# Performance work log

Measured on AMD Instinct MI355X. Metric: run time of the kernel, lower is better.

Reference implementation:

```python
import jax, jax.numpy as jnp
import numpy as np

N_NODES = 100000
N_EDGES = 1600000
D_IN = 64
D_OUT = 64


def setup_inputs() -> dict:
    key = jax.random.key(0)
    k1, k2, k3, k4, k5 = jax.random.split(key, 5)
    x = jax.random.normal(k1, (N_NODES, D_IN), dtype=jnp.float32)
    edge_src = jax.random.randint(k2, (N_EDGES,), 0, N_NODES, dtype=jnp.int32)
    edge_dst = jax.random.randint(k3, (N_EDGES,), 0, N_NODES, dtype=jnp.int32)
    edge_val = jnp.ones((N_EDGES,), dtype=jnp.float32)
    stdv = 1.0 / np.sqrt(D_OUT)
    weight = jax.random.uniform(k4, (D_IN, D_OUT), minval=-stdv, maxval=stdv, dtype=jnp.float32)
    epsilon = jnp.ones((1,), dtype=jnp.float32)
    bias = jax.random.uniform(k5, (D_OUT,), minval=-stdv, maxval=stdv, dtype=jnp.float32)
    return {"x": x, "edge_src": edge_src, "edge_dst": edge_dst,
            "edge_val": edge_val, "weight": weight, "epsilon": epsilon, "bias": bias}


def reference(x, edge_src, edge_dst, edge_val, weight, epsilon, bias):
    # spmm(adj, x): row i of adj gathers neighbors -> segment_sum over edge_src
    # adj[i, j] = edge_val for edge (src=i, dst=j)
    msgs = edge_val[:, None] * x[edge_dst]            # [E, D_in]
    agg = jax.ops.segment_sum(msgs, edge_src, num_segments=N_NODES)  # [N, D_in]
    # epsilon * eye(N) @ x == epsilon * x (avoid O(N^2) identity)
    rep = agg + epsilon * x                            # [N, D_in]
    out = rep @ weight + bias                          # [N, D_out]
    return out, rep
```

## Files before the change

### kernel.cpp

```cpp
#include <hip/hip_runtime.h>
#include <hip/hip_fp16.h>

#define N_NODES 100000
#define N_EDGES 1600000
#define D 64

#define NB 391
#define BLKA 391
#define EPB 4096
#define GST 400

#define WS_GHIST   0
#define WS_G       156416
#define WS_ROWPTR  156832
#define WS_PAIRSU  256864
#define WS_XH      1856864

__global__ __launch_bounds__(512) void k_hist_cvt(
    const int* __restrict__ esrc, const float* __restrict__ x,
    int* __restrict__ ghist, uint2* __restrict__ xh2)
{
    __shared__ int h[NB];
    int t = threadIdx.x, blk = blockIdx.x;
    if (t < NB) h[t] = 0;
    __syncthreads();
    int base = blk * EPB;
    #pragma unroll
    for (int i = 0; i < 2; ++i) {
        int e0 = base + i * 2048 + t * 4;
        if (e0 < N_EDGES) {
            int4 s4 = *(const int4*)(esrc + e0);
            atomicAdd(&h[s4.x >> 8], 1);
            atomicAdd(&h[s4.y >> 8], 1);
            atomicAdd(&h[s4.z >> 8], 1);
            atomicAdd(&h[s4.w >> 8], 1);
        }
    }
    {
        const float4* x4 = (const float4*)x;
        #pragma unroll
        for (int i = 0; i < 8; ++i) {
            int f = blk * 4096 + i * 512 + t;
            if (f < N_NODES * (D / 4)) {
                float4 v = x4[f];
                uint2 o;
                o.x = (unsigned int)__half_as_ushort(__float2half_rn(v.x)) |
                      ((unsigned int)__half_as_ushort(__float2half_rn(v.y)) << 16);
                o.y = (unsigned int)__half_as_ushort(__float2half_rn(v.z)) |
                      ((unsigned int)__half_as_ushort(__float2half_rn(v.w)) << 16);
                xh2[f] = o;
            }
        }
    }
    __syncthreads();
    if (t < NB) ghist[blk * GST + t] = h[t];
}

__global__ __launch_bounds__(512) void k_scatter(
    const int* __restrict__ esrc, const int* __restrict__ edst,
    const float* __restrict__ eval_, const int* __restrict__ ghist,
    int* __restrict__ G, int2* __restrict__ tpairs)
{
    __shared__ int base[NB];
    __shared__ int wsum[8];
    int t = threadIdx.x, blk = blockIdx.x;
    int lane = t & 63, wid = t >> 6;

    int tot = 0, P = 0;
    if (t < NB) {
        int c = 0;
        for (; c + 16 <= BLKA; c += 16) {
            int v[16];
            #pragma unroll
            for (int k = 0; k < 16; ++k) v[k] = ghist[(c + k) * GST + t];
            #pragma unroll
            for (int k = 0; k < 16; ++k) {
                tot += v[k];
                P += ((c + k) < blk) ? v[k] : 0;
            }
        }
        for (; c < BLKA; ++c) {
            int v = ghist[c * GST + t];
            tot += v;
            P += (c < blk) ? v : 0;
        }
    }
    int s = tot;
    #pragma unroll
    for (int off = 1; off < 64; off <<= 1) {
        int y = __shfl_up(s, off, 64);
        if (lane >= off) s += y;
    }
    if (lane == 63) wsum[wid] = s;
    __syncthreads();
    if (t == 0) {
        int r = 0;
        #pragma unroll
        for (int k = 0; k < 8; ++k) { int v = wsum[k]; wsum[k] = r; r += v; }
    }
    __syncthreads();
    int Gv = wsum[wid] + s - tot;
    if (t < NB) {
        base[t] = Gv + P;
        if (blk == 0) {
            G[t] = Gv;
            if (t == NB - 1) G[NB] = Gv + tot;
        }
    }
    __syncthreads();

    int eb = blk * EPB;
    #pragma unroll
    for (int i = 0; i < 2; ++i) {
        int e0 = eb + i * 2048 + t * 4;
        if (e0 < N_EDGES) {
            int4 s4 = *(const int4*)(esrc + e0);
            int4 d4 = *(const int4*)(edst + e0);
            float4 v4 = *(const float4*)(eval_ + e0);
            int p0 = atomicAdd(&base[s4.x >> 8], 1);
            int p1 = atomicAdd(&base[s4.y >> 8], 1);
            int p2 = atomicAdd(&base[s4.z >> 8], 1);
            int p3 = atomicAdd(&base[s4.w >> 8], 1);
            tpairs[p0] = make_int2(((s4.x & 255) << 17) | d4.x, __float_as_int(v4.x));
            tpairs[p1] = make_int2(((s4.y & 255) << 17) | d4.y, __float_as_int(v4.y));
            tpairs[p2] = make_int2(((s4.z & 255) << 17) | d4.z, __float_as_int(v4.z));
            tpairs[p3] = make_int2(((s4.w & 255) << 17) | d4.w, __float_as_int(v4.w));
        }
    }
}

__global__ __launch_bounds__(512) void k_build(
    const int2* __restrict__ tpairs, const int* __restrict__ G,
    int* __restrict__ row_ptr, unsigned int* __restrict__ pairsu)
{
    __shared__ int hist[256], cursor[256], wsum4[4];
    int b = blockIdx.x, t = threadIdx.x;
    int s_begin = G[b];
    int s_end   = G[b + 1];
    if (t < 256) hist[t] = 0;
    __syncthreads();
    #pragma unroll 4
    for (int pos = s_begin + t; pos < s_end; pos += 512)
        atomicAdd(&hist[(tpairs[pos].x >> 17) & 255], 1);
    __syncthreads();
    int lane = t & 63, wid = t >> 6;
    if (t < 256) {
        int v = hist[t], s = v;
        #pragma unroll
        for (int off = 1; off < 64; off <<= 1) {
            int y = __shfl_up(s, off, 64);
            if (lane >= off) s += y;
        }
        if (lane == 63) wsum4[wid] = s;
        __syncthreads();
        if (t == 0) {
            int r = 0;
            #pragma unroll
            for (int k = 0; k < 4; ++k) { int w = wsum4[k]; wsum4[k] = r; r += w; }
        }
        __syncthreads();
        int excl = wsum4[wid] + s - v;
        cursor[t] = excl;
        int node = (b << 8) + t;
        if (node <= N_NODES) row_ptr[node] = s_begin + excl;
    } else {
        __syncthreads();
        __syncthreads();
    }
    __syncthreads();
    #pragma unroll 4
    for (int pos = s_begin + t; pos < s_end; pos += 512) {
        int2 pv = tpairs[pos];
        int k = (pv.x >> 17) & 255;
        int p = atomicAdd(&cursor[k], 1);
        unsigned int dst = (unsigned int)pv.x & 0x1FFFFu;
        unsigned int hb = (unsigned int)__half_as_ushort(
            __float2half_rn(__int_as_float(pv.y)));
        pairsu[s_begin + p] = (dst << 15) | (hb >> 1);
    }
}

#define GATHER_BLOCKS 2048

__global__ __launch_bounds__(256) void k_gather(
    const uint4* __restrict__ xh4, const int* __restrict__ row_ptr,
    const unsigned int* __restrict__ pairsu, const float* __restrict__ epsilon,
    float* __restrict__ rep)
{
    int w = (blockIdx.x * 256 + threadIdx.x) >> 6;
    int nw = gridDim.x * 4;
    int lane = threadIdx.x & 63;
    int sub = lane >> 3;
    int h8 = lane & 7;
    float eps = epsilon[0];

    int r0 = (int)((long long)w * N_NODES / nw);
    int r1 = (int)((long long)(w + 1) * N_NODES / nw);

    for (int row = r0; row < r1; ++row) {
        int start = __builtin_amdgcn_readfirstlane(row_ptr[row]);
        int end   = __builtin_amdgcn_readfirstlane(row_ptr[row + 1]);
        float4 accA = make_float4(0.f, 0.f, 0.f, 0.f);
        float4 accB = make_float4(0.f, 0.f, 0.f, 0.f);
        for (int j = start; j < end; j += 32) {
            unsigned int pk[4]; uint4 a[4];
            #pragma unroll
            for (int u = 0; u < 4; ++u) {
                int e = j + u * 8 + sub;
                pk[u] = (e < end) ? pairsu[e] : 0u;
            }
            #pragma unroll
            for (int u = 0; u < 4; ++u)
                a[u] = xh4[(size_t)(pk[u] >> 15) * 8 + h8];
            #pragma unroll
            for (int u = 0; u < 4; ++u) {
                unsigned short hb = (unsigned short)((pk[u] & 0x7FFFu) << 1);
                float vv = __half2float(__ushort_as_half(hb));
                float2 f0 = __half22float2(*reinterpret_cast<const __half2*>(&a[u].x));
                float2 f1 = __half22float2(*reinterpret_cast<const __half2*>(&a[u].y));
                float2 f2 = __half22float2(*reinterpret_cast<const __half2*>(&a[u].z));
                float2 f3 = __half22float2(*reinterpret_cast<const __half2*>(&a[u].w));
                accA.x += vv * f0.x; accA.y += vv * f0.y;
                accA.z += vv * f1.x; accA.w += vv * f1.y;
                accB.x += vv * f2.x; accB.y += vv * f2.y;
                accB.z += vv * f3.x; accB.w += vv * f3.y;
            }
        }
        #pragma unroll
        for (int off = 8; off <= 32; off <<= 1) {
            accA.x += __shfl_xor(accA.x, off, 64);
            accA.y += __shfl_xor(accA.y, off, 64);
            accA.z += __shfl_xor(accA.z, off, 64);
            accA.w += __shfl_xor(accA.w, off, 64);
            accB.x += __shfl_xor(accB.x, off, 64);
            accB.y += __shfl_xor(accB.y, off, 64);
            accB.z += __shfl_xor(accB.z, off, 64);
            accB.w += __shfl_xor(accB.w, off, 64);
        }
        if (lane < 8) {
            uint4 xr = xh4[(size_t)row * 8 + lane];
            float2 x0 = __half22float2(*reinterpret_cast<const __half2*>(&xr.x));
            float2 x1 = __half22float2(*reinterpret_cast<const __half2*>(&xr.y));
            float2 x2 = __half22float2(*reinterpret_cast<const __half2*>(&xr.z));
            float2 x3 = __half22float2(*reinterpret_cast<const __half2*>(&xr.w));
            float4* r4 = (float4*)rep;
            r4[(size_t)row * 16 + lane * 2] =
                make_float4(accA.x + eps * x0.x, accA.y + eps * x0.y,
                            accA.z + eps * x1.x, accA.w + eps * x1.y);
            r4[(size_t)row * 16 + lane * 2 + 1] =
                make_float4(accB.x + eps * x2.x, accB.y + eps * x2.y,
                            accB.z + eps * x3.x, accB.w + eps * x3.y);
        }
    }
}

#define GEMM_TM 64
__global__ __launch_bounds__(256) void k_gemm(
    const float* __restrict__ rep, const float* __restrict__ weight,
    const float* __restrict__ bias, float* __restrict__ out)
{
    __shared__ float rep_s[GEMM_TM * 68];
    __shared__ float Ws[D * D];
    int t = threadIdx.x;
    {
        const float4* w4 = (const float4*)weight;
        float4* s4 = (float4*)Ws;
        #pragma unroll
        for (int i = 0; i < (D * D / 4) / 256; ++i)
            s4[t + i * 256] = w4[t + i * 256];
    }
    int row0 = blockIdx.x * GEMM_TM;
    {
        const float4* r4 = (const float4*)rep;
        #pragma unroll
        for (int i = 0; i < 4; ++i) {
            int f = t + i * 256;
            int rr = f >> 4, kk4 = f & 15;
            float4 v = (row0 + rr < N_NODES) ? r4[(size_t)(row0 + rr) * 16 + kk4]
                                             : make_float4(0.f, 0.f, 0.f, 0.f);
            rep_s[rr * 68 + kk4 * 4 + 0] = v.x;
            rep_s[rr * 68 + kk4 * 4 + 1] = v.y;
            rep_s[rr * 68 + kk4 * 4 + 2] = v.z;
            rep_s[rr * 68 + kk4 * 4 + 3] = v.w;
        }
    }
    __syncthreads();

    int tx = t & 15, ty = t >> 4;
    float4 b4 = ((const float4*)bias)[tx];
    float acc[4][4];
    #pragma unroll
    for (int i = 0; i < 4; ++i) {
        acc[i][0] = b4.x; acc[i][1] = b4.y; acc[i][2] = b4.z; acc[i][3] = b4.w;
    }
    #pragma unroll 4
    for (int k4 = 0; k4 < 16; ++k4) {
        float4 rv[4];
        #pragma unroll
        for (int i = 0; i < 4; ++i)
            rv[i] = *(const float4*)&rep_s[(ty * 4 + i) * 68 + k4 * 4];
        #pragma unroll
        for (int kk = 0; kk < 4; ++kk) {
            float4 wv = *(const float4*)&Ws[(k4 * 4 + kk) * D + tx * 4];
            #pragma unroll
            for (int i = 0; i < 4; ++i) {
                float r = ((const float*)&rv[i])[kk];
                acc[i][0] += r * wv.x;
                acc[i][1] += r * wv.y;
                acc[i][2] += r * wv.z;
                acc[i][3] += r * wv.w;
            }
        }
    }
    #pragma unroll
    for (int i = 0; i < 4; ++i) {
        int row = row0 + ty * 4 + i;
        if (row < N_NODES)
            *(float4*)&out[(size_t)row * D + tx * 4] =
                make_float4(acc[i][0], acc[i][1], acc[i][2], acc[i][3]);
    }
}

extern "C" void kernel_launch(void* const* d_in, const int* in_sizes, int n_in,
                              void* d_out, int out_size, void* d_ws, size_t ws_size,
                              hipStream_t stream) {
    const float* x    = (const float*)d_in[0];
    const int*   esrc = (const int*)  d_in[1];
    const int*   edst = (const int*)  d_in[2];
    const float* ev   = (const float*)d_in[3];
    const float* w    = (const float*)d_in[4];
    const float* eps  = (const float*)d_in[5];
    const float* bias = (const float*)d_in[6];

    float* out = (float*)d_out;
    float* rep = out + (size_t)N_NODES * D;

    int* ws       = (int*)d_ws;
    int* ghist    = ws + WS_GHIST;
    int* G        = ws + WS_G;
    int* row_ptr  = ws + WS_ROWPTR;
    unsigned int* pairsu = (unsigned int*)(ws + WS_PAIRSU);
    uint2* xh2    = (uint2*)(ws + WS_XH);
    uint4* xh4    = (uint4*)(ws + WS_XH);
    int2* tpairs  = (int2*)rep;

    k_hist_cvt<<<BLKA, 512, 0, stream>>>(esrc, x, ghist, xh2);
    k_scatter<<<BLKA, 512, 0, stream>>>(esrc, edst, ev, ghist, G, tpairs);
    k_build<<<NB, 512, 0, stream>>>(tpairs, G, row_ptr, pairsu);
    k_gather<<<GATHER_BLOCKS, 256, 0, stream>>>(xh4, row_ptr, pairsu, eps, rep);
    k_gemm<<<(N_NODES + GEMM_TM - 1) / GEMM_TM, 256, 0, stream>>>(rep, w, bias, out);
}
```

Baseline: 199.4 us.

## Double block size for CSR build kernels and edge-balance gather row ranges

The three CSR construction kernels now use 1024-thread blocks that cover the same per-block work in a single pass, replacing the 512-thread two-iteration loops. The scan synchronisation in k_build is restructured so every thread reaches the same barriers. k_gather now splits work by equal edge counts per wavefront, using a binary search over row_ptr, instead of equal row counts. This is meant to balance load across warps, at the cost of a binary search per wavefront and lower occupancy flexibility for the larger blocks.

```diff
diff --git a/kernel.cpp b/kernel.cpp
--- a/kernel.cpp
+++ b/kernel.cpp
@@ -16,7 +16,8 @@
 #define WS_PAIRSU  256864
 #define WS_XH      1856864
 
-__global__ __launch_bounds__(512) void k_hist_cvt(
+
+__global__ __launch_bounds__(1024) void k_hist_cvt(
     const int* __restrict__ esrc, const float* __restrict__ x,
     int* __restrict__ ghist, uint2* __restrict__ xh2)
 {
@@ -24,10 +25,8 @@
     int t = threadIdx.x, blk = blockIdx.x;
     if (t < NB) h[t] = 0;
     __syncthreads();
-    int base = blk * EPB;
-    #pragma unroll
-    for (int i = 0; i < 2; ++i) {
-        int e0 = base + i * 2048 + t * 4;
+    {
+        int e0 = blk * EPB + t * 4;
         if (e0 < N_EDGES) {
             int4 s4 = *(const int4*)(esrc + e0);
             atomicAdd(&h[s4.x >> 8], 1);
@@ -39,8 +38,8 @@
     {
         const float4* x4 = (const float4*)x;
         #pragma unroll
-        for (int i = 0; i < 8; ++i) {
-            int f = blk * 4096 + i * 512 + t;
+        for (int i = 0; i < 4; ++i) {
+            int f = blk * 4096 + i * 1024 + t;
             if (f < N_NODES * (D / 4)) {
                 float4 v = x4[f];
                 uint2 o;
@@ -56,13 +55,13 @@
     if (t < NB) ghist[blk * GST + t] = h[t];
 }
 
-__global__ __launch_bounds__(512) void k_scatter(
+__global__ __launch_bounds__(1024) void k_scatter(
     const int* __restrict__ esrc, const int* __restrict__ edst,
     const float* __restrict__ eval_, const int* __restrict__ ghist,
     int* __restrict__ G, int2* __restrict__ tpairs)
 {
     __shared__ int base[NB];
-    __shared__ int wsum[8];
+    __shared__ int wsum[16];
     int t = threadIdx.x, blk = blockIdx.x;
     int lane = t & 63, wid = t >> 6;
 
@@ -96,7 +95,7 @@
     if (t == 0) {
         int r = 0;
         #pragma unroll
-        for (int k = 0; k < 8; ++k) { int v = wsum[k]; wsum[k] = r; r += v; }
+        for (int k = 0; k < 16; ++k) { int v = wsum[k]; wsum[k] = r; r += v; }
     }
     __syncthreads();
     int Gv = wsum[wid] + s - tot;
@@ -109,10 +108,8 @@
     }
     __syncthreads();
 
-    int eb = blk * EPB;
-    #pragma unroll
-    for (int i = 0; i < 2; ++i) {
-        int e0 = eb + i * 2048 + t * 4;
+    {
+        int e0 = blk * EPB + t * 4;
         if (e0 < N_EDGES) {
             int4 s4 = *(const int4*)(esrc + e0);
             int4 d4 = *(const int4*)(edst + e0);
@@ -129,7 +126,7 @@
     }
 }
 
-__global__ __launch_bounds__(512) void k_build(
+__global__ __launch_bounds__(1024) void k_build(
     const int2* __restrict__ tpairs, const int* __restrict__ G,
     int* __restrict__ row_ptr, unsigned int* __restrict__ pairsu)
 {
@@ -139,37 +136,35 @@
     int s_end   = G[b + 1];
     if (t < 256) hist[t] = 0;
     __syncthreads();
-    #pragma unroll 4
-    for (int pos = s_begin + t; pos < s_end; pos += 512)
+    for (int pos = s_begin + t; pos < s_end; pos += 1024)
         atomicAdd(&hist[(tpairs[pos].x >> 17) & 255], 1);
     __syncthreads();
     int lane = t & 63, wid = t >> 6;
+    int v = 0, s = 0;
     if (t < 256) {
-        int v = hist[t], s = v;
+        v = hist[t]; s = v;
         #pragma unroll
         for (int off = 1; off < 64; off <<= 1) {
             int y = __shfl_up(s, off, 64);
             if (lane >= off) s += y;
         }
         if (lane == 63) wsum4[wid] = s;
-        __syncthreads();
-        if (t == 0) {
-            int r = 0;
-            #pragma unroll
-            for (int k = 0; k < 4; ++k) { int w = wsum4[k]; wsum4[k] = r; r += w; }
-        }
-        __syncthreads();
+    }
+    __syncthreads();
+    if (t == 0) {
+        int r = 0;
+        #pragma unroll
+        for (int k = 0; k < 4; ++k) { int w = wsum4[k]; wsum4[k] = r; r += w; }
+    }
+    __syncthreads();
+    if (t < 256) {
         int excl = wsum4[wid] + s - v;
         cursor[t] = excl;
         int node = (b << 8) + t;
         if (node <= N_NODES) row_ptr[node] = s_begin + excl;
-    } else {
-        __syncthreads();
-        __syncthreads();
-    }
-    __syncthreads();
-    #pragma unroll 4
-    for (int pos = s_begin + t; pos < s_end; pos += 512) {
+    }
+    __syncthreads();
+    for (int pos = s_begin + t; pos < s_end; pos += 1024) {
         int2 pv = tpairs[pos];
         int k = (pv.x >> 17) & 255;
         int p = atomicAdd(&cursor[k], 1);
@@ -182,6 +177,15 @@
 
 #define GATHER_BLOCKS 2048
 
+__device__ __forceinline__ int lb_rowptr(const int* __restrict__ rp, int target) {
+    int lo = 0, hi = N_NODES;
+    while (lo < hi) {
+        int mid = (lo + hi) >> 1;
+        if (rp[mid] < target) lo = mid + 1; else hi = mid;
+    }
+    return lo;
+}
+
 __global__ __launch_bounds__(256) void k_gather(
     const uint4* __restrict__ xh4, const int* __restrict__ row_ptr,
     const unsigned int* __restrict__ pairsu, const float* __restrict__ epsilon,
@@ -194,8 +198,10 @@
     int h8 = lane & 7;
     float eps = epsilon[0];
 
-    int r0 = (int)((long long)w * N_NODES / nw);
-    int r1 = (int)((long long)(w + 1) * N_NODES / nw);
+    int elo = (int)((long long)N_EDGES * w / nw);
+    int ehi = (int)((long long)N_EDGES * (w + 1) / nw);
+    int r0 = lb_rowptr(row_ptr, elo);
+    int r1 = (w == nw - 1) ? N_NODES : lb_rowptr(row_ptr, ehi);
 
     for (int row = r0; row < r1; ++row) {
         int start = __builtin_amdgcn_readfirstlane(row_ptr[row]);
@@ -344,9 +350,9 @@
     uint4* xh4    = (uint4*)(ws + WS_XH);
     int2* tpairs  = (int2*)rep;
 
-    k_hist_cvt<<<BLKA, 512, 0, stream>>>(esrc, x, ghist, xh2);
-    k_scatter<<<BLKA, 512, 0, stream>>>(esrc, edst, ev, ghist, G, tpairs);
-    k_build<<<NB, 512, 0, stream>>>(tpairs, G, row_ptr, pairsu);
+    k_hist_cvt<<<BLKA, 1024, 0, stream>>>(esrc, x, ghist, xh2);
+    k_scatter<<<BLKA, 1024, 0, stream>>>(esrc, edst, ev, ghist, G, tpairs);
+    k_build<<<NB, 1024, 0, stream>>>(tpairs, G, row_ptr, pairsu);
     k_gather<<<GATHER_BLOCKS, 256, 0, stream>>>(xh4, row_ptr, pairsu, eps, rep);
     k_gemm<<<(N_NODES + GEMM_TM - 1) / GEMM_TM, 256, 0, stream>>>(rep, w, bias, out);
 }
```

Measured after the change: 209.8 us. 5.2% more time.
